# Kernel optimization log

Hardware: AMD Instinct MI355X
Metric: run time of the kernel (lower is better)

## Reference

```python
import jax, jax.numpy as jnp
import numpy as np

R = 2          # total_rel
N = 6144       # total_ent / num nodes
H1 = 256       # layer 1 out
H2 = 256       # layer 2 out


def setup_inputs() -> dict:
    key = jax.random.key(0)
    k_adj, k_w1, k_c1, k_w2, k_c2 = jax.random.split(key, 5)
    adj = jax.random.uniform(k_adj, (R, N, N), dtype=jnp.float32)
    bw1 = jax.random.normal(k_w1, (R, N, H1), dtype=jnp.float32) * (1.0 / np.sqrt(N))
    bc1 = jax.random.normal(k_c1, (R, R), dtype=jnp.float32)
    bw2 = jax.random.normal(k_w2, (R, H1, H2), dtype=jnp.float32) * (1.0 / np.sqrt(H1))
    bc2 = jax.random.normal(k_c2, (R, R), dtype=jnp.float32)
    return {"adj": adj, "bw1": bw1, "bc1": bc1, "bw2": bw2, "bc2": bc2}


def _layer_weights(coeff, basis):
    # (R, n_basis) x (n_basis, in, out) -> (R*in, out)
    w = jnp.einsum('ij,jmn->imn', coeff, basis)
    return w.reshape(w.shape[0] * w.shape[1], w.shape[2])


def reference(adj, bw1, bc1, bw2, bc2):
    # --- layer 1: node_init is None -> features are dense adjacencies ---
    w1 = _layer_weights(bc1, bw1)                        # (R*N, H1)
    # cat([adj[0], adj[1]], axis=1) == transpose+reshape  (N, R*N)
    tmp1 = adj.transpose(1, 0, 2).reshape(N, R * N)
    out1 = tmp1 @ w1                                     # (N, H1)

    # --- layer 2: relu then per-relation spmm + basis matmul ---
    x = jax.nn.relu(out1)
    w2 = _layer_weights(bc2, bw2)                        # (R*H1, H2)
    # cat([adj[r] @ x for r], axis=1) as one einsum       (N, R*H1)
    tmp2 = jnp.einsum('rij,jd->ird', adj, x).reshape(N, R * H1)
    out2 = tmp2 @ w2                                     # (N, H2)

    final_rep = jnp.concatenate([out1, out2], axis=1)    # (N, H1+H2)
    final_rep = jnp.sum(final_rep, axis=0).reshape(-1, H1 + H2)  # (1, H1+H2)
    return (out2, final_rep)
```

## Files before the change

kernel.cpp:

```cpp
#include <hip/hip_runtime.h>


#define NN 6144
#define HH 256
#define SPLIT 8
#define KCHUNK 1536
#define KSTEPS 24

typedef __attribute__((ext_vector_type(4))) float f32x4;
typedef __attribute__((ext_vector_type(8))) unsigned short u16x8;
typedef __attribute__((ext_vector_type(4))) unsigned short u16x4;

__device__ __forceinline__ unsigned short f2bf(float f) {
  unsigned int u = __float_as_uint(f);
  u += 0x7FFFu + ((u >> 16) & 1u);
  return (unsigned short)(u >> 16);
}
__device__ __forceinline__ float bf2f(unsigned short h) {
  return __uint_as_float(((unsigned int)h) << 16);
}

__device__ __forceinline__ void mfma_bf16(f32x4& d, u16x8 a, u16x8 b) {
  asm("v_mfma_f32_16x16x32_bf16 %0, %1, %2, %0" : "+v"(d) : "v"(a), "v"(b));
}

__global__ void wgen_kernel(const float* __restrict__ basis,
                            const float* __restrict__ bc,
                            unsigned short* __restrict__ outw,
                            int tilesPerR, int jdim)
{
  __shared__ unsigned short wt[64][265];
  const int t  = blockIdx.x;
  const int r  = t / tilesPerR;
  const int jt = t % tilesPerR;
  const float c0 = bc[r * 2 + 0];
  const float c1 = bc[r * 2 + 1];
  const int tid = threadIdx.x;
  const float* b0 = basis + (size_t)jt * 64 * HH;
  const float* b1 = basis + (size_t)jdim * HH + (size_t)jt * 64 * HH;
#pragma unroll
  for (int k = 0; k < 16; ++k) {
    int idx = tid + k * 256;
    int row = idx >> 6;
    int c4  = (idx & 63) * 4;
    f32x4 v0 = *(const f32x4*)(b0 + (size_t)row * HH + c4);
    f32x4 v1 = *(const f32x4*)(b1 + (size_t)row * HH + c4);
    wt[row][c4 + 0] = f2bf(c0 * v0.x + c1 * v1.x);
    wt[row][c4 + 1] = f2bf(c0 * v0.y + c1 * v1.y);
    wt[row][c4 + 2] = f2bf(c0 * v0.z + c1 * v1.z);
    wt[row][c4 + 3] = f2bf(c0 * v0.w + c1 * v1.w);
  }
  __syncthreads();
#pragma unroll
  for (int k = 0; k < 8; ++k) {
    int chunk = tid + k * 256;
    int h  = chunk >> 3;
    int sp = chunk & 7;
    int j0 = (sp ^ (h & 7)) * 8;
    u16x8 v;
#pragma unroll
    for (int e = 0; e < 8; ++e) v[e] = wt[j0 + e][h];
    *(u16x8*)(outw + ((size_t)t * 2048 + chunk) * 8) = v;
  }
}

__global__ __launch_bounds__(256, 3) void gemm_adj_kernel(
    const float* __restrict__ adj, const unsigned short* __restrict__ Bws,
    unsigned short* __restrict__ Pp)
{
  __shared__ __align__(16) unsigned short Alds[64 * 64];
  __shared__ __align__(16) unsigned short Blds[256 * 64];
  const int tid  = threadIdx.x;
  const int lane = tid & 63;
  const int wave = tid >> 6;
  const int mb = blockIdx.x;
  const int s  = blockIdx.y;
  const int i0 = mb * 64;
  const int kbase = s * KCHUNK;
  const int rrel  = kbase / NN;
  const int jb    = kbase % NN;
  const int tBase = kbase / 64;

  const float* aRow = adj + (size_t)rrel * NN * NN
                      + (size_t)(i0 + (tid >> 4)) * NN + jb + (tid & 15) * 4;
  const unsigned short* bBase = Bws + (size_t)tBase * 2048 * 8 + (size_t)tid * 8;

  f32x4 acc[4][4];
#pragma unroll
  for (int m = 0; m < 4; ++m)
#pragma unroll
    for (int n = 0; n < 4; ++n) acc[m][n] = (f32x4){0.f, 0.f, 0.f, 0.f};

  f32x4 av[4];
  u16x8 bv[8];

#define LOADK(KK) do {                                                        \
    _Pragma("unroll")                                                         \
    for (int it = 0; it < 4; ++it)                                            \
      av[it] = *(const f32x4*)(aRow + (size_t)it * 16 * NN + (KK) * 64);      \
    _Pragma("unroll")                                                         \
    for (int c = 0; c < 8; ++c)                                               \
      bv[c] = *(const u16x8*)(bBase + (size_t)(KK) * 2048 * 8 + c * 256 * 8); \
  } while (0)

  LOADK(0);

  for (int kk = 0; kk < KSTEPS; ++kk) {
    __syncthreads();
#pragma unroll
    for (int it = 0; it < 4; ++it) {
      int row = (tid >> 4) + it * 16;
      int off = ((tid & 15) * 8) ^ ((row & 7) << 4);
      u16x4 w;
      w[0] = f2bf(av[it].x); w[1] = f2bf(av[it].y);
      w[2] = f2bf(av[it].z); w[3] = f2bf(av[it].w);
      *(u16x4*)((char*)Alds + row * 128 + off) = w;
    }
#pragma unroll
    for (int c = 0; c < 8; ++c)
      *(u16x8*)(Blds + ((size_t)c * 256 + tid) * 8) = bv[c];
    __syncthreads();
    if (kk + 1 < KSTEPS) LOADK(kk + 1);
#pragma unroll
    for (int ks = 0; ks < 2; ++ks) {
      u16x8 af[4], bfr[4];
#pragma unroll
      for (int m = 0; m < 4; ++m) {
        int row = m * 16 + (lane & 15);
        int off = (ks * 64 + ((lane >> 4) << 4)) ^ ((row & 7) << 4);
        af[m] = *(const u16x8*)((const char*)Alds + row * 128 + off);
      }
#pragma unroll
      for (int n = 0; n < 4; ++n) {
        int row = wave * 64 + n * 16 + (lane & 15);
        int off = (ks * 64 + ((lane >> 4) << 4)) ^ ((row & 7) << 4);
        bfr[n] = *(const u16x8*)((const char*)Blds + row * 128 + off);
      }
#pragma unroll
      for (int m = 0; m < 4; ++m)
#pragma unroll
        for (int n = 0; n < 4; ++n)
          mfma_bf16(acc[m][n], af[m], bfr[n]);
    }
  }
#undef LOADK
  unsigned short* P = Pp + ((size_t)s * NN + i0) * HH;
#pragma unroll
  for (int m = 0; m < 4; ++m)
#pragma unroll
    for (int n = 0; n < 4; ++n) {
      int col = wave * 64 + n * 16 + (lane & 15);
#pragma unroll
      for (int q = 0; q < 4; ++q) {
        int row = m * 16 + ((lane >> 4) << 2) + q;
        P[(size_t)row * HH + col] = f2bf(acc[m][n][q]);
      }
    }
}

__global__ __launch_bounds__(256, 2) void gemm_y_kernel(
    const unsigned short* __restrict__ xws, const unsigned short* __restrict__ w2ws,
    unsigned short* __restrict__ B2ws)
{
  __shared__ __align__(16) unsigned short Alds[64 * 64];
  __shared__ __align__(16) unsigned short Blds[256 * 64];
  const int tid  = threadIdx.x;
  const int lane = tid & 63;
  const int wave = tid >> 6;
  const int mb = blockIdx.x;
  const int r  = blockIdx.y;

  f32x4 acc[4][4];
#pragma unroll
  for (int m = 0; m < 4; ++m)
#pragma unroll
    for (int n = 0; n < 4; ++n) acc[m][n] = (f32x4){0.f, 0.f, 0.f, 0.f};

  for (int dt = 0; dt < 4; ++dt) {
    u16x8 avv[2];
    avv[0] = *(const u16x8*)(xws + (((size_t)(mb * 4 + dt)) * 512 + tid) * 8);
    avv[1] = *(const u16x8*)(xws + (((size_t)(mb * 4 + dt)) * 512 + 256 + tid) * 8);
    u16x8 bv[8];
#pragma unroll
    for (int c = 0; c < 8; ++c)
      bv[c] = *(const u16x8*)(w2ws + (((size_t)(r * 4 + dt)) * 2048 + c * 256 + tid) * 8);
    __syncthreads();
    *(u16x8*)(Alds + (size_t)tid * 8) = avv[0];
    *(u16x8*)(Alds + ((size_t)256 + tid) * 8) = avv[1];
#pragma unroll
    for (int c = 0; c < 8; ++c)
      *(u16x8*)(Blds + ((size_t)c * 256 + tid) * 8) = bv[c];
    __syncthreads();
#pragma unroll
    for (int ks = 0; ks < 2; ++ks) {
      u16x8 af[4], bfr[4];
#pragma unroll
      for (int m = 0; m < 4; ++m) {
        int row = m * 16 + (lane & 15);
        int off = (ks * 64 + ((lane >> 4) << 4)) ^ ((row & 7) << 4);
        af[m] = *(const u16x8*)((const char*)Alds + row * 128 + off);
      }
#pragma unroll
      for (int n = 0; n < 4; ++n) {
        int row = wave * 64 + n * 16 + (lane & 15);
        int off = (ks * 64 + ((lane >> 4) << 4)) ^ ((row & 7) << 4);
        bfr[n] = *(const u16x8*)((const char*)Blds + row * 128 + off);
      }
#pragma unroll
      for (int m = 0; m < 4; ++m)
#pragma unroll
        for (int n = 0; n < 4; ++n)
          mfma_bf16(acc[m][n], af[m], bfr[n]);
    }
  }
  const int tg = r * 96 + mb;
#pragma unroll
  for (int m = 0; m < 4; ++m) {
    int scont = m * 2 + ((lane >> 4) >> 1);
    int e0    = ((lane >> 4) & 1) * 4;
#pragma unroll
    for (int n = 0; n < 4; ++n) {
      int h   = wave * 64 + n * 16 + (lane & 15);
      int pos = scont ^ (h & 7);
      u16x4 v;
      v[0] = f2bf(acc[m][n][0]); v[1] = f2bf(acc[m][n][1]);
      v[2] = f2bf(acc[m][n][2]); v[3] = f2bf(acc[m][n][3]);
      *(u16x4*)(B2ws + (((size_t)tg * 2048 + h * 8 + pos) * 8 + e0)) = v;
    }
  }
}

__global__ void reduce1_kernel(const unsigned short* __restrict__ Pp,
                               unsigned short* __restrict__ xws,
                               float* __restrict__ fin)
{
  __shared__ float csm[8][256];
  const int tid = threadIdx.x;
  const int b   = blockIdx.x;
  const int hc  = tid & 31;
  const int rg  = tid >> 5;
  const int dt    = hc >> 3;
  const int scont = hc & 7;
  float cs[8] = {0.f, 0.f, 0.f, 0.f, 0.f, 0.f, 0.f, 0.f};
  for (int k = 0; k < 8; ++k) {
    int i = b * 64 + rg + k * 8;
    float sv[8] = {0.f, 0.f, 0.f, 0.f, 0.f, 0.f, 0.f, 0.f};
#pragma unroll
    for (int s = 0; s < SPLIT; ++s) {
      u16x8 v = *(const u16x8*)(Pp + ((size_t)s * NN + i) * HH + hc * 8);
#pragma unroll
      for (int e = 0; e < 8; ++e) sv[e] += bf2f(v[e]);
    }
    u16x8 xv;
#pragma unroll
    for (int e = 0; e < 8; ++e) {
      cs[e] += sv[e];
      xv[e] = f2bf(fmaxf(sv[e], 0.f));
    }
    int pos = scont ^ (i & 7);
    *(u16x8*)(xws + (((size_t)(b * 4 + dt)) * 512 + (i & 63) * 8 + pos) * 8) = xv;
  }
#pragma unroll
  for (int e = 0; e < 8; ++e) csm[rg][hc * 8 + e] = cs[e];
  __syncthreads();
  float v = 0.f;
#pragma unroll
  for (int r8 = 0; r8 < 8; ++r8) v += csm[r8][tid];
  atomicAdd(&fin[tid], v);
}

__global__ void reduce2_kernel(const unsigned short* __restrict__ Pp,
                               float* __restrict__ outp,
                               float* __restrict__ fin)
{
  __shared__ float csm[8][256];
  const int tid = threadIdx.x;
  const int b   = blockIdx.x;
  const int hc  = tid & 31;
  const int rg  = tid >> 5;
  float cs[8] = {0.f, 0.f, 0.f, 0.f, 0.f, 0.f, 0.f, 0.f};
  for (int k = 0; k < 8; ++k) {
    int i = b * 64 + rg + k * 8;
    float sv[8] = {0.f, 0.f, 0.f, 0.f, 0.f, 0.f, 0.f, 0.f};
#pragma unroll
    for (int s = 0; s < SPLIT; ++s) {
      u16x8 v = *(const u16x8*)(Pp + ((size_t)s * NN + i) * HH + hc * 8);
#pragma unroll
      for (int e = 0; e < 8; ++e) sv[e] += bf2f(v[e]);
    }
    float* o = outp + (size_t)i * HH + hc * 8;
    *(f32x4*)o = (f32x4){sv[0], sv[1], sv[2], sv[3]};
    *(f32x4*)(o + 4) = (f32x4){sv[4], sv[5], sv[6], sv[7]};
#pragma unroll
    for (int e = 0; e < 8; ++e) cs[e] += sv[e];
  }
#pragma unroll
  for (int e = 0; e < 8; ++e) csm[rg][hc * 8 + e] = cs[e];
  __syncthreads();
  float v = 0.f;
#pragma unroll
  for (int r8 = 0; r8 < 8; ++r8) v += csm[r8][tid];
  atomicAdd(&fin[256 + tid], v);
}

__global__ void zero_fin_kernel(float* fin) {
  fin[blockIdx.x * 256 + threadIdx.x] = 0.f;
}

extern "C" void kernel_launch(void* const* d_in, const int* in_sizes, int n_in,
                              void* d_out, int out_size, void* d_ws, size_t ws_size,
                              hipStream_t stream)
{
  const float* adj = (const float*)d_in[0];
  const float* bw1 = (const float*)d_in[1];
  const float* bc1 = (const float*)d_in[2];
  const float* bw2 = (const float*)d_in[3];
  const float* bc2 = (const float*)d_in[4];
  float* out2 = (float*)d_out;
  float* fin  = (float*)d_out + (size_t)NN * HH;

  char* ws = (char*)d_ws;
  unsigned short* Pp   = (unsigned short*)(ws + 0);
  unsigned short* B1ws = (unsigned short*)(ws + 25165824);
  unsigned short* B2ws = (unsigned short*)(ws + 31457280);
  unsigned short* xws  = (unsigned short*)(ws + 37748736);
  unsigned short* w2ws = (unsigned short*)(ws + 40894464);

  zero_fin_kernel<<<2, 256, 0, stream>>>(fin);
  wgen_kernel<<<192, 256, 0, stream>>>(bw1, bc1, B1ws, 96, NN);
  gemm_adj_kernel<<<dim3(96, SPLIT), 256, 0, stream>>>(adj, B1ws, Pp);
  reduce1_kernel<<<96, 256, 0, stream>>>(Pp, xws, fin);
  wgen_kernel<<<8, 256, 0, stream>>>(bw2, bc2, w2ws, 4, HH);
  gemm_y_kernel<<<dim3(96, 2), 256, 0, stream>>>(xws, w2ws, B2ws);
  gemm_adj_kernel<<<dim3(96, SPLIT), 256, 0, stream>>>(adj, B2ws, Pp);
  reduce2_kernel<<<96, 256, 0, stream>>>(Pp, out2, fin);
}
```

Before: 203.7 us.

## Double-buffer LDS in adjacency GEMM with direct global-to-LDS B loads

Reworks the main adjacency GEMM loop to use two LDS buffers for A and B, prefetching two k-steps ahead with one barrier per step instead of two. B tiles are now copied straight into LDS via global_load_lds rather than passing through registers. A is loaded as 8 floats per thread in a new row/column mapping. The aim is to overlap the fp32 adjacency streaming with MFMA compute and cut register pressure for B. In exchange, LDS use doubles and the launch bound drops occupancy from 3 to 2 blocks per CU.

```diff
diff --git a/kernel.cpp b/kernel.cpp
--- a/kernel.cpp
+++ b/kernel.cpp
@@ -22,6 +22,13 @@
 
 __device__ __forceinline__ void mfma_bf16(f32x4& d, u16x8 a, u16x8 b) {
   asm("v_mfma_f32_16x16x32_bf16 %0, %1, %2, %0" : "+v"(d) : "v"(a), "v"(b));
+}
+
+__device__ __forceinline__ void gll16(const unsigned short* g, unsigned short* l) {
+  __builtin_amdgcn_global_load_lds(
+      (const __attribute__((address_space(1))) unsigned int*)g,
+      (__attribute__((address_space(3))) unsigned int*)l,
+      16, 0, 0);
 }
 
 __global__ void wgen_kernel(const float* __restrict__ basis,
@@ -64,12 +71,12 @@
   }
 }
 
-__global__ __launch_bounds__(256, 3) void gemm_adj_kernel(
+__global__ __launch_bounds__(256, 2) void gemm_adj_kernel(
     const float* __restrict__ adj, const unsigned short* __restrict__ Bws,
     unsigned short* __restrict__ Pp)
 {
-  __shared__ __align__(16) unsigned short Alds[64 * 64];
-  __shared__ __align__(16) unsigned short Blds[256 * 64];
+  __shared__ __align__(16) unsigned short Alds[2][64 * 64];
+  __shared__ __align__(16) unsigned short Blds[2][256 * 64];
   const int tid  = threadIdx.x;
   const int lane = tid & 63;
   const int wave = tid >> 6;
@@ -81,9 +88,11 @@
   const int jb    = kbase % NN;
   const int tBase = kbase / 64;
 
-  const float* aRow = adj + (size_t)rrel * NN * NN
-                      + (size_t)(i0 + (tid >> 4)) * NN + jb + (tid & 15) * 4;
-  const unsigned short* bBase = Bws + (size_t)tBase * 2048 * 8 + (size_t)tid * 8;
+  const int arow = tid >> 3;
+  const int acol = (tid & 7) * 8;
+  const float* aPtr = adj + (size_t)rrel * NN * NN
+                      + (size_t)(i0 + arow) * NN + jb + acol;
+  const unsigned short* bPtr = Bws + (size_t)tBase * 2048 * 8 + (size_t)tid * 8;
 
   f32x4 acc[4][4];
 #pragma unroll
@@ -91,59 +100,83 @@
 #pragma unroll
     for (int n = 0; n < 4; ++n) acc[m][n] = (f32x4){0.f, 0.f, 0.f, 0.f};
 
-  f32x4 av[4];
-  u16x8 bv[8];
-
-#define LOADK(KK) do {                                                        \
-    _Pragma("unroll")                                                         \
-    for (int it = 0; it < 4; ++it)                                            \
-      av[it] = *(const f32x4*)(aRow + (size_t)it * 16 * NN + (KK) * 64);      \
-    _Pragma("unroll")                                                         \
-    for (int c = 0; c < 8; ++c)                                               \
-      bv[c] = *(const u16x8*)(bBase + (size_t)(KK) * 2048 * 8 + c * 256 * 8); \
-  } while (0)
-
-  LOADK(0);
-
-  for (int kk = 0; kk < KSTEPS; ++kk) {
+  f32x4 av0[2][2], av1[2][2];
+
+#define ISSUE_A(SET, KK) do {                                                  \
+    _Pragma("unroll")                                                          \
+    for (int it = 0; it < 2; ++it) {                                           \
+      SET[it][0] = *(const f32x4*)(aPtr + (size_t)it * 32 * NN + (KK) * 64);   \
+      SET[it][1] = *(const f32x4*)(aPtr + (size_t)it * 32 * NN + (KK) * 64 + 4);\
+    } } while (0)
+
+#define ISSUE_B(BUF, KK) do {                                                  \
+    _Pragma("unroll")                                                          \
+    for (int c = 0; c < 8; ++c)                                                \
+      gll16(bPtr + (size_t)(KK) * 2048 * 8 + c * 256 * 8,                      \
+            (unsigned short*)((char*)Blds[BUF] + ((size_t)c * 256 + tid) * 16)); \
+    } while (0)
+
+#define STAGE_A(SET, BUF) do {                                                 \
+    _Pragma("unroll")                                                          \
+    for (int it = 0; it < 2; ++it) {                                           \
+      int row = arow + it * 32;                                                \
+      u16x8 w;                                                                 \
+      w[0] = f2bf(SET[it][0].x); w[1] = f2bf(SET[it][0].y);                    \
+      w[2] = f2bf(SET[it][0].z); w[3] = f2bf(SET[it][0].w);                    \
+      w[4] = f2bf(SET[it][1].x); w[5] = f2bf(SET[it][1].y);                    \
+      w[6] = f2bf(SET[it][1].z); w[7] = f2bf(SET[it][1].w);                    \
+      *(u16x8*)((char*)Alds[BUF] + row * 128 +                                 \
+                ((((tid & 7) ^ (row & 7))) << 4)) = w;                         \
+    } } while (0)
+
+#define COMPUTE(BUF) do {                                                      \
+    _Pragma("unroll")                                                          \
+    for (int ks = 0; ks < 2; ++ks) {                                           \
+      u16x8 af[4], bfr[4];                                                     \
+      _Pragma("unroll")                                                        \
+      for (int m = 0; m < 4; ++m) {                                            \
+        int row = m * 16 + (lane & 15);                                        \
+        int off = (ks * 64 + ((lane >> 4) << 4)) ^ ((row & 7) << 4);           \
+        af[m] = *(const u16x8*)((const char*)Alds[BUF] + row * 128 + off);     \
+      }                                                                        \
+      _Pragma("unroll")                                                        \
+      for (int n = 0; n < 4; ++n) {                                            \
+        int row = wave * 64 + n * 16 + (lane & 15);                            \
+        int off = (ks * 64 + ((lane >> 4) << 4)) ^ ((row & 7) << 4);           \
+        bfr[n] = *(const u16x8*)((const char*)Blds[BUF] + row * 128 + off);    \
+      }                                                                        \
+      _Pragma("unroll")                                                        \
+      for (int m = 0; m < 4; ++m)                                              \
+        _Pragma("unroll")                                                      \
+        for (int n = 0; n < 4; ++n)                                            \
+          mfma_bf16(acc[m][n], af[m], bfr[n]);                                 \
+    } } while (0)
+
+  ISSUE_B(0, 0);
+  ISSUE_A(av0, 0);
+  ISSUE_A(av1, 1);
+  STAGE_A(av0, 0);
+  __syncthreads();
+
+  for (int kk = 0; kk < KSTEPS; kk += 2) {
+    ISSUE_B(1, kk + 1);
+    if (kk + 2 < KSTEPS) ISSUE_A(av0, kk + 2);
+    COMPUTE(0);
+    STAGE_A(av1, 1);
     __syncthreads();
-#pragma unroll
-    for (int it = 0; it < 4; ++it) {
-      int row = (tid >> 4) + it * 16;
-      int off = ((tid & 15) * 8) ^ ((row & 7) << 4);
-      u16x4 w;
-      w[0] = f2bf(av[it].x); w[1] = f2bf(av[it].y);
-      w[2] = f2bf(av[it].z); w[3] = f2bf(av[it].w);
-      *(u16x4*)((char*)Alds + row * 128 + off) = w;
-    }
-#pragma unroll
-    for (int c = 0; c < 8; ++c)
-      *(u16x8*)(Blds + ((size_t)c * 256 + tid) * 8) = bv[c];
+    if (kk + 2 < KSTEPS) {
+      ISSUE_B(0, kk + 2);
+      if (kk + 3 < KSTEPS) ISSUE_A(av1, kk + 3);
+    }
+    COMPUTE(1);
+    if (kk + 2 < KSTEPS) STAGE_A(av0, 0);
     __syncthreads();
-    if (kk + 1 < KSTEPS) LOADK(kk + 1);
-#pragma unroll
-    for (int ks = 0; ks < 2; ++ks) {
-      u16x8 af[4], bfr[4];
-#pragma unroll
-      for (int m = 0; m < 4; ++m) {
-        int row = m * 16 + (lane & 15);
-        int off = (ks * 64 + ((lane >> 4) << 4)) ^ ((row & 7) << 4);
-        af[m] = *(const u16x8*)((const char*)Alds + row * 128 + off);
-      }
-#pragma unroll
-      for (int n = 0; n < 4; ++n) {
-        int row = wave * 64 + n * 16 + (lane & 15);
-        int off = (ks * 64 + ((lane >> 4) << 4)) ^ ((row & 7) << 4);
-        bfr[n] = *(const u16x8*)((const char*)Blds + row * 128 + off);
-      }
-#pragma unroll
-      for (int m = 0; m < 4; ++m)
-#pragma unroll
-        for (int n = 0; n < 4; ++n)
-          mfma_bf16(acc[m][n], af[m], bfr[n]);
-    }
-  }
-#undef LOADK
+  }
+#undef ISSUE_A
+#undef ISSUE_B
+#undef STAGE_A
+#undef COMPUTE
+
   unsigned short* P = Pp + ((size_t)s * NN + i0) * HH;
 #pragma unroll
   for (int m = 0; m < 4; ++m)
```

Result: slower. 228.0 us (+11.9%).
